# Optimization experiments

Measured on AMD Instinct MI355X. Metric: run time of the kernel, lower is better.

Reference implementation:

```python
import jax, jax.numpy as jnp
import numpy as np

B, A, C, L, NH, SCALE = 1, 5, 64, 4, 8, 2
H = W = 24
S = 2 * C
KS = 5


def layernorm(x, g, b, eps=1e-5):
    m = x.mean(-1, keepdims=True)
    v = ((x - m) ** 2).mean(-1, keepdims=True)
    return (x - m) * jax.lax.rsqrt(v + eps) * g + b


def pe_1d(n, d):
    # PositionEncoding: temperature**(2*(i//2)/d), sin of even cols then cos of odd cols
    g = jnp.arange(d, dtype=jnp.float32)
    g = 10000.0 ** (2.0 * jnp.floor(g / 2.0) / d)
    p = jnp.arange(n, dtype=jnp.float32)[:, None] / g[None, :]
    return jnp.concatenate([jnp.sin(p[:, 0::2]), jnp.cos(p[:, 1::2])], axis=1)  # [n, d]


def mha(qk, v, in_w, out_w, nh, mask=None):
    # qk, v: [Lq, Bt, D]; torch nn.MultiheadAttention, bias-free, q=k=qk, value=v
    Lq, Bt, D = qk.shape
    dh = D // nh
    wq, wk, wv = jnp.split(in_w, 3, axis=0)
    q = (qk @ wq.T).reshape(Lq, Bt, nh, dh)
    k = (qk @ wk.T).reshape(Lq, Bt, nh, dh)
    vv = (v @ wv.T).reshape(Lq, Bt, nh, dh)
    s = jnp.einsum('lbhd,mbhd->bhlm', q, k) / jnp.sqrt(jnp.float32(dh))
    if mask is not None:
        s = s + mask
    a = jax.nn.softmax(s, axis=-1)
    o = jnp.einsum('bhlm,mbhd->lbhd', a, vv).reshape(Lq, Bt, D)
    return o @ out_w.T


def unfold3x3(x):
    # F.unfold(k=3, pad=1).permute(2,0,1): [N,c,h,w] -> [h*w, N, 9c] (c, kh, kw ordering)
    N, c, h, w = x.shape
    xp = jnp.pad(x, ((0, 0), (0, 0), (1, 1), (1, 1)))
    p = jnp.stack([xp[:, :, i:i + h, j:j + w] for i in range(3) for j in range(3)], axis=2)
    return p.reshape(N, c * 9, h * w).transpose(2, 0, 1)


def conv_hw(x5, w):
    # Conv3d kernel (1,3,3) pad (0,1,1): 2D conv per angular view
    Bc, Ci, Aa, h, w_ = x5.shape
    y = jax.lax.conv_general_dilated(
        x5.transpose(0, 2, 1, 3, 4).reshape(Bc * Aa, Ci, h, w_), w, (1, 1), ((1, 1), (1, 1)),
        dimension_numbers=('NCHW', 'OIHW', 'NCHW'))
    return y.reshape(Bc, Aa, w.shape[0], h, w_).transpose(0, 2, 1, 3, 4)


def window_mask(h, w, k):
    # SpaTrans.gen_mask: additive -inf outside a k x k local window
    kl, kr = k // 2, k - k // 2
    i = jnp.arange(h)
    j = jnp.arange(w)
    mh = (i[None, :] >= i[:, None] - kl) & (i[None, :] < i[:, None] + kr)
    mw = (j[None, :] >= j[:, None] - kl) & (j[None, :] < j[:, None] + kr)
    m = (mh[:, None, :, None] & mw[None, :, None, :]).reshape(h * w, h * w)
    return jnp.where(m, 0.0, -jnp.inf).astype(jnp.float32)


def setup_inputs() -> dict:
    key = jax.random.key(0)
    ks = iter(jax.random.split(key, 64))
    def nrm(shape, s=0.02):
        return jax.random.normal(next(ks), shape, dtype=jnp.float32) * s
    d = {}
    d['lr'] = jax.random.normal(next(ks), (B, 1, A * H, A * W), dtype=jnp.float32)
    Hh, Wh = H * SCALE, W * SCALE
    ch = -1.0 + (2.0 * jnp.arange(Hh, dtype=jnp.float32) + 1.0) / Hh
    cw = -1.0 + (2.0 * jnp.arange(Wh, dtype=jnp.float32) + 1.0) / Wh
    g = jnp.stack(jnp.meshgrid(ch, cw, indexing='ij'), axis=-1).reshape(-1, 2)
    d['coord'] = jnp.broadcast_to(g, (B, Hh * Wh, 2))
    d['conv0_w'] = nrm((C, 1, 3, 3), 0.1)
    d['convi_w'] = nrm((3, C, C, 3, 3), 0.05)
    d['ang_ln_g'] = jnp.ones((L, C)); d['ang_ln_b'] = jnp.zeros((L, C))
    d['ang_in'] = nrm((L, 3 * C, C)); d['ang_out'] = nrm((L, C, C))
    d['ang_ff_g'] = jnp.ones((L, C)); d['ang_ff_b'] = jnp.zeros((L, C))
    d['ang_w1'] = nrm((L, 2 * C, C)); d['ang_w2'] = nrm((L, C, 2 * C))
    d['spa_mlp'] = nrm((L, S, 9 * C))
    d['spa_ln_g'] = jnp.ones((L, S)); d['spa_ln_b'] = jnp.zeros((L, S))
    d['spa_in'] = nrm((L, 3 * S, S)); d['spa_out'] = nrm((L, S, S))
    d['spa_ff_g'] = jnp.ones((L, S)); d['spa_ff_b'] = jnp.zeros((L, S))
    d['spa_w1'] = nrm((L, 2 * S, S)); d['spa_w2'] = nrm((L, S, 2 * S))
    d['spa_lin'] = nrm((L, C, S))
    IN = A * A * C + 2 + 2 * A * A
    d['imp_w0'] = nrm((320, IN)); d['imp_b0'] = jnp.zeros((320,))
    d['imp_w1'] = nrm((320, 320)); d['imp_b1'] = jnp.zeros((320,))
    d['imp_w2'] = nrm((3 * A * A, 320)); d['imp_b2'] = jnp.zeros((3 * A * A,))
    return d


def reference(lr, coord, conv0_w, convi_w, ang_ln_g, ang_ln_b, ang_in, ang_out,
              ang_ff_g, ang_ff_b, ang_w1, ang_w2, spa_mlp, spa_ln_g, spa_ln_b,
              spa_in, spa_out, spa_ff_g, spa_ff_b, spa_w1, spa_w2, spa_lin,
              imp_w0, imp_b0, imp_w1, imp_b1, imp_w2, imp_b2):
    Bn = lr.shape[0]
    # 'b c (a1 h) (a2 w) -> b c (a1 a2) h w'
    x = lr.reshape(Bn, 1, A, H, A, W).transpose(0, 1, 2, 4, 3, 5).reshape(Bn, 1, A * A, H, W)
    spa_pe_img = ((pe_1d(H, C)[:, None, :] + pe_1d(W, C)[None, :, :]) * 0.5).transpose(2, 0, 1)[None]  # [1,C,h,w]
    ang_pe = pe_1d(A * A, C)[:, None, :]  # [A^2,1,C]
    buf = conv_hw(x, conv0_w)
    t = buf
    for i in range(3):
        t = jax.nn.leaky_relu(conv_hw(t, convi_w[i]), 0.2)
    buf = t + buf
    mask = window_mask(H, W, KS)
    blk = buf
    for l in range(L):
        # ---- AngTrans: tokens [A^2, B*h*w, C]
        tok = blk.transpose(2, 0, 3, 4, 1).reshape(A * A, Bn * H * W, C)
        tn = layernorm(tok + ang_pe, ang_ln_g[l], ang_ln_b[l])
        tok = mha(tn, tok, ang_in[l], ang_out[l], NH) + tok
        ff = layernorm(tok, ang_ff_g[l], ang_ff_b[l])
        tok = jax.nn.relu(ff @ ang_w1[l].T) @ ang_w2[l].T + tok
        blk = tok.reshape(A * A, Bn, H, W, C).transpose(1, 4, 0, 2, 3)
        # ---- SpaTrans: tokens [h*w, B*A^2, 2C] with local-window mask
        xb = blk.transpose(0, 2, 1, 3, 4).reshape(Bn * A * A, C, H, W)
        tok = unfold3x3(xb) @ spa_mlp[l].T
        pe_tok = unfold3x3(spa_pe_img) @ spa_mlp[l].T
        tn = layernorm(tok + pe_tok, spa_ln_g[l], spa_ln_b[l])
        tok = mha(tn, tok, spa_in[l], spa_out[l], NH, mask) + tok
        ff = layernorm(tok, spa_ff_g[l], spa_ff_b[l])
        tok = jax.nn.relu(ff @ spa_w1[l].T) @ spa_w2[l].T + tok
        t5 = tok.reshape(H, W, Bn, A * A, S).transpose(2, 4, 3, 0, 1)  # b s a h w
        blk = jnp.einsum('os,bsahw->boahw', spa_lin[l], t5)  # 1x1x1 Conv3d
    buf = blk + buf
    # 'b c (a1 a2) h w -> b c (a1 h) (a2 w)'
    feat_lr = buf.reshape(Bn, C, A, A, H, W).transpose(0, 1, 2, 4, 3, 5).reshape(Bn, C, A * H, A * W)
    Hh, Wh = H * SCALE, W * SCALE
    # per-view bilinear upsample (align_corners=False)
    v = feat_lr.reshape(Bn, C, A, H, A, W).transpose(0, 2, 4, 1, 3, 5).reshape(Bn * A * A, C, H, W)
    v = jax.image.resize(v, (Bn * A * A, C, Hh, Wh), method='bilinear')
    feat_hr = v.reshape(Bn, A, A, C, Hh, Wh).transpose(0, 4, 5, 1, 2, 3).reshape(Bn, Hh, Wh, A * A * C)
    # nearest grid_sample of LR cell-center coords -> relative coord
    c_ = jnp.clip(coord + 1e-6, -1 + 1e-6, 1 - 1e-6)
    ih = jnp.clip(jnp.round(((c_[..., 0] + 1) * H - 1) / 2), 0, H - 1)
    iw = jnp.clip(jnp.round(((c_[..., 1] + 1) * W - 1) / 2), 0, W - 1)
    qh = -1.0 + (2.0 * ih + 1.0) / H
    qw = -1.0 + (2.0 * iw + 1.0) / W
    rel = jnp.stack([(coord[..., 0] - qh) * H, (coord[..., 1] - qw) * W], axis=-1).reshape(Bn, Hh, Wh, 2)
    au = 0.5 + jnp.arange(A, dtype=jnp.float32)  # make_coord ranges [0,A]
    ca = jnp.stack(jnp.meshgrid(au, au, indexing='ij'), axis=-1).reshape(-1)
    ca = jnp.broadcast_to(ca, (Bn, Hh, Wh, 2 * A * A))
    inp = jnp.concatenate([feat_hr, rel, ca], axis=-1)
    h0 = jax.nn.relu(inp @ imp_w0.T + imp_b0)
    h1 = jax.nn.relu(h0 @ imp_w1.T + imp_b1)
    o = h1 @ imp_w2.T + imp_b2
    # 'b h w (a1 a2 c) -> b c (a1 h) (a2 w)', c=3
    return o.reshape(Bn, Hh, Wh, A, A, 3).transpose(0, 5, 3, 1, 4, 2).reshape(Bn, 3, A * Hh, A * Wh)
```

## Files before the change

kernel.cpp:

```cpp
#include <hip/hip_runtime.h>
#include <math.h>

typedef short  s16x4 __attribute__((ext_vector_type(4)));
typedef short  s16x8 __attribute__((ext_vector_type(8)));
typedef float  f32x4 __attribute__((ext_vector_type(4)));

static const size_t PE25_  = 0;
static const size_t SPAPE_ = 2048;
static const size_t X_     = 38912;
static const size_t CAV_   = 53312;
static const size_t PETOK_ = 54272;
static const size_t W9C_   = 349184;
static const size_t W9S_   = 459776;
static const size_t BUF_   = 754688;
static const size_t BLK_   = 1676288;
static const size_t ATOK_  = 2597888;
static const size_t TNF_   = 3519488;
static const size_t STOK_  = 4441088;
static const size_t STOK2_ = 6284288;
static const size_t AO_    = 8127488;
static const size_t QKV_   = 9970688;
static const size_t WS_FLOATS = 15500288;
static const size_t T0_ = QKV_ + 2764800;
static const size_t T1_ = T0_ + 921600;
static const size_t ZP_ = QKV_;
static const size_t H0_ = STOK_;
static const size_t H1_ = STOK2_;

__device__ inline ushort f2bf(float x) {
  unsigned u = __float_as_uint(x);
  u += 0x7fffu + ((u >> 16) & 1u);
  return (ushort)(u >> 16);
}
__device__ inline float bf2f(ushort h) { return __uint_as_float(((unsigned)h) << 16); }

__device__ inline void store_split(char* p, f32x4 v) {
  s16x4 hi, lo;
  #pragma unroll
  for (int e = 0; e < 4; ++e) {
    float x = v[e];
    ushort h = f2bf(x);
    ushort l = f2bf(x - bf2f(h));
    hi[e] = (short)h; lo[e] = (short)l;
  }
  *(s16x4*)p = hi;
  *(s16x4*)(p + 1024) = lo;
}

__device__ inline void scatter_split(char* base, int rr, int c6, float v) {
  ushort hi = f2bf(v);
  ushort lo = f2bf(v - bf2f(hi));
  int ks = c6 >> 5, kh = (c6 >> 4) & 1, k4 = (c6 >> 2) & 3;
  int lane2 = (k4 >> 1)*32 + ((rr & 15) << 1) + (k4 & 1);
  int byt = (((rr >> 4)*2 + ks) << 11) + (kh << 9) + (lane2 << 3) + (c6 & 3)*2;
  *(ushort*)(base + byt) = hi;
  *(ushort*)(base + byt + 1024) = lo;
}

__device__ inline void ld_bf16x16(const ushort* p, float* dst) {
  s16x8 a = *(const s16x8*)p;
  s16x8 b = *(const s16x8*)(p + 8);
  #pragma unroll
  for (int e = 0; e < 8; ++e) { dst[e] = bf2f((ushort)a[e]); dst[8 + e] = bf2f((ushort)b[e]); }
}

__device__ inline void slot_decode(int i, int wave, int lane,
                                   int& row, int& kof, int& wo) {
  int idx = (i << 2) + wave;
  int msub = idx >> 2, ks = (idx >> 1) & 1, kh = idx & 1;
  int rsub = (lane >> 1) & 15;
  int ksub = ((lane >> 5) << 3) + ((lane & 1) << 2);
  row = (msub << 4) + rsub;
  kof = (ks << 5) + (kh << 4) + ksub;
  wo = ((msub * 2 + ks) << 11) + (kh << 9) + (lane << 3);
}

__device__ inline void mfma_step(const char* ldsA, const char* ldsB, int lane,
                                 int wr, int wc, f32x4 acc[2][2]) {
  #pragma unroll
  for (int ks = 0; ks < 2; ++ks) {
    s16x8 ah[2], al[2], bh[2], bl[2];
    #pragma unroll
    for (int i = 0; i < 2; ++i) {
      const char* pa = ldsA + (((wr*2 + i)*2 + ks) << 11) + (lane << 4);
      ah[i] = *(const s16x8*)pa;
      al[i] = *(const s16x8*)(pa + 1024);
      const char* pb = ldsB + (((wc*2 + i)*2 + ks) << 11) + (lane << 4);
      bh[i] = *(const s16x8*)pb;
      bl[i] = *(const s16x8*)(pb + 1024);
    }
    #pragma unroll
    for (int i = 0; i < 2; ++i) {
      #pragma unroll
      for (int j = 0; j < 2; ++j) {
        acc[i][j] = __builtin_amdgcn_mfma_f32_16x16x32_bf16(ah[i], bh[j], acc[i][j], 0, 0, 0);
        acc[i][j] = __builtin_amdgcn_mfma_f32_16x16x32_bf16(ah[i], bl[j], acc[i][j], 0, 0, 0);
        acc[i][j] = __builtin_amdgcn_mfma_f32_16x16x32_bf16(al[i], bh[j], acc[i][j], 0, 0, 0);
      }
    }
  }
}

__device__ inline void epilogue(f32x4 acc[2][2], const float* bias, const float* res,
                                float* out, int N, int m0, int n0,
                                int wr, int wc, int lane, int act) {
  int colb = n0 + wc*32 + (lane & 15);
  int rowb = m0 + wr*32 + ((lane >> 4) << 2);
  #pragma unroll
  for (int j = 0; j < 2; ++j) {
    int cc = colb + j*16;
    if (cc >= N) continue;
    float bv = bias ? bias[cc] : 0.f;
    #pragma unroll
    for (int i = 0; i < 2; ++i) {
      #pragma unroll
      for (int r = 0; r < 4; ++r) {
        int rr = rowb + i*16 + r;
        float v = acc[i][j][r] + bv;
        if (act == 1) v = fmaxf(v, 0.f);
        else if (act == 2) v = v > 0.f ? v : 0.2f*v;
        if (res) v += res[(long)rr*N + cc];
        if (act == 3) {
          int hh = rr / 48, ww2 = rr % 48, q = cc / 3, ch = cc % 3;
          out[ch*57600 + ((q/5)*48 + hh)*240 + (q%5)*48 + ww2] = v;
        } else if (act == 4) {
          ((ushort*)out)[(long)rr*N + cc] = f2bf(v);
        } else {
          out[(long)rr*N + cc] = v;
        }
      }
    }
  }
}

template<int K, int LN>
__global__ __launch_bounds__(256) void mgemm3_k(
    const float* __restrict__ A, const float* __restrict__ A2, int nsplit,
    const float* __restrict__ pe, int pe_mode,
    const float* __restrict__ g, const float* __restrict__ bb,
    const float* __restrict__ W, const float* __restrict__ bias,
    const float* __restrict__ res, float* __restrict__ out,
    int N, int act, int Mreal, int Mpad) {
  constexpr int NCH = K / 64;
  __shared__ char Apl[NCH * 16384];
  __shared__ char Bp[16384];
  __shared__ float sw_[4][64][2];
  __shared__ float sf_[64][2];
  int bid = blockIdx.x;
  int m = bid % Mpad, nt = bid / Mpad;
  if (m >= Mreal) return;
  int m0 = m*64, n0 = nt*64;
  int t = threadIdx.x, lane = t & 63, wave = t >> 6;
  int wr = wave >> 1, wc = wave & 1;
  bool use_norm = LN && (n0 < nsplit);

  if (LN && use_norm) {
    f32x4 rv[NCH][4];
    float sA[4], sQ[4];
    #pragma unroll
    for (int i = 0; i < 4; ++i) { sA[i] = 0.f; sQ[i] = 0.f; }
    #pragma unroll
    for (int ch = 0; ch < NCH; ++ch)
      #pragma unroll
      for (int i = 0; i < 4; ++i) {
        int row, kof, wo;
        slot_decode(i, wave, lane, row, kof, wo);
        int gk = ch*64 + kof;
        f32x4 av = *(const f32x4*)&A[(long)(m0 + row)*K + gk];
        if (pe_mode == 0)      av += *(const f32x4*)&pe[(long)(m0/576)*K + gk];
        else if (pe_mode == 1) av += *(const f32x4*)&pe[(long)(m0%576 + row)*K + gk];
        rv[ch][i] = av;
        #pragma unroll
        for (int e = 0; e < 4; ++e) { sA[i] += av[e]; sQ[i] = fmaf(av[e], av[e], sQ[i]); }
      }
    #pragma unroll
    for (int i = 0; i < 4; ++i) {
      float s = sA[i], q = sQ[i];
      s += __shfl_xor(s, 1, 64);  q += __shfl_xor(q, 1, 64);
      s += __shfl_xor(s, 32, 64); q += __shfl_xor(q, 32, 64);
      if ((lane & 1) == 0 && lane < 32) {
        int row = i*16 + (lane >> 1);
        sw_[wave][row][0] = s; sw_[wave][row][1] = q;
      }
    }
    __syncthreads();
    if (t < 64) {
      float s = sw_[0][t][0] + sw_[1][t][0] + sw_[2][t][0] + sw_[3][t][0];
      float q = sw_[0][t][1] + sw_[1][t][1] + sw_[2][t][1] + sw_[3][t][1];
      float mean = s / K, var = q / K - mean*mean;
      sf_[t][0] = mean; sf_[t][1] = rsqrtf(var + 1e-5f);
    }
    __syncthreads();
    #pragma unroll
    for (int ch = 0; ch < NCH; ++ch)
      #pragma unroll
      for (int i = 0; i < 4; ++i) {
        int row, kof, wo;
        slot_decode(i, wave, lane, row, kof, wo);
        int gk = ch*64 + kof;
        float mean = sf_[row][0], rstd = sf_[row][1];
        f32x4 gv = *(const f32x4*)&g[gk];
        f32x4 bv = *(const f32x4*)&bb[gk];
        f32x4 nv;
        #pragma unroll
        for (int e = 0; e < 4; ++e) nv[e] = (rv[ch][i][e] - mean)*rstd*gv[e] + bv[e];
        store_split(Apl + ch*16384 + wo, nv);
      }
  } else {
    const float* As = LN ? A2 : A;
    #pragma unroll
    for (int ch = 0; ch < NCH; ++ch)
      #pragma unroll
      for (int i = 0; i < 4; ++i) {
        int row, kof, wo;
        slot_decode(i, wave, lane, row, kof, wo);
        f32x4 av = *(const f32x4*)&As[(long)(m0 + row)*K + ch*64 + kof];
        store_split(Apl + ch*16384 + wo, av);
      }
  }

  f32x4 pb[4];
  #pragma unroll
  for (int i = 0; i < 4; ++i) {
    int row, kof, wo;
    slot_decode(i, wave, lane, row, kof, wo);
    int br = n0 + row;
    pb[i] = (br < N) ? *(const f32x4*)&W[(long)br*K + kof] : (f32x4){0.f,0.f,0.f,0.f};
  }
  __syncthreads();
  f32x4 acc[2][2];
  #pragma unroll
  for (int i = 0; i < 2; ++i)
    #pragma unroll
    for (int j = 0; j < 2; ++j) acc[i][j] = (f32x4){0.f,0.f,0.f,0.f};
  for (int ch = 0; ch < NCH; ++ch) {
    #pragma unroll
    for (int i = 0; i < 4; ++i) {
      int row, kof, wo;
      slot_decode(i, wave, lane, row, kof, wo);
      store_split(Bp + wo, pb[i]);
    }
    __syncthreads();
    if (ch + 1 < NCH) {
      #pragma unroll
      for (int i = 0; i < 4; ++i) {
        int row, kof, wo;
        slot_decode(i, wave, lane, row, kof, wo);
        int br = n0 + row;
        pb[i] = (br < N) ? *(const f32x4*)&W[(long)br*K + (ch+1)*64 + kof]
                         : (f32x4){0.f,0.f,0.f,0.f};
      }
    }
    mfma_step(Apl + ch*16384, Bp, lane, wr, wc, acc);
    if (ch + 1 < NCH) __syncthreads();
  }
  epilogue(acc, bias, res, out, N, m0, n0, wr, wc, lane, act);
}

__global__ __launch_bounds__(256) void cgemm3_k(
    const float* __restrict__ in, const float* __restrict__ W9, long wstride,
    const float* __restrict__ res, float* __restrict__ out, long ostride,
    int N, int act, int Mreal, int Mpad) {
  __shared__ float halo[144 * 68];
  __shared__ char Ap[16384], Bp[16384];
  int bid = blockIdx.x;
  int m = bid % Mpad, nt = bid / Mpad;
  if (m >= Mreal) return;
  int ly = blockIdx.y;
  W9  += (long)ly * wstride;
  out += (long)ly * ostride;
  int m0 = m*64, n0 = nt*64;
  int a = m0 / 576, off = m0 % 576;
  int h_lo = off/24 - 1, h_hi = (off + 63)/24 + 1;
  int RH = h_hi - h_lo + 1;
  int t = threadIdx.x, lane = t & 63, wave = t >> 6;
  int wr = wave >> 1, wc = wave & 1;
  for (int sidx = t; sidx < RH*24*16; sidx += 256) {
    int tokr = sidx >> 4, c4 = (sidx & 15) << 2;
    int h = h_lo + tokr/24, w = tokr % 24;
    f32x4 v = {0.f,0.f,0.f,0.f};
    if ((unsigned)h < 24u) v = *(const f32x4*)&in[(long)(a*576 + h*24 + w)*64 + c4];
    *(f32x4*)&halo[tokr*68 + c4] = v;
  }
  f32x4 pb[4];
  #pragma unroll
  for (int i = 0; i < 4; ++i) {
    int row, kof, wo;
    slot_decode(i, wave, lane, row, kof, wo);
    int br = n0 + row;
    pb[i] = (br < N) ? *(const f32x4*)&W9[(long)br*64 + kof] : (f32x4){0.f,0.f,0.f,0.f};
  }
  __syncthreads();
  f32x4 acc[2][2];
  #pragma unroll
  for (int i = 0; i < 2; ++i)
    #pragma unroll
    for (int j = 0; j < 2; ++j) acc[i][j] = (f32x4){0.f,0.f,0.f,0.f};
  for (int ij = 0; ij < 9; ++ij) {
    int di = ij/3 - 1, dj = ij%3 - 1;
    #pragma unroll
    for (int i = 0; i < 4; ++i) {
      int row, kof, wo;
      slot_decode(i, wave, lane, row, kof, wo);
      int tok = off + row;
      int h2 = tok/24 + di, w2 = tok%24 + dj;
      f32x4 v = {0.f,0.f,0.f,0.f};
      if ((unsigned)h2 < 24u && (unsigned)w2 < 24u)
        v = *(const f32x4*)&halo[((h2 - h_lo)*24 + w2)*68 + kof];
      store_split(Ap + wo, v);
      store_split(Bp + wo, pb[i]);
    }
    __syncthreads();
    if (ij < 8) {
      #pragma unroll
      for (int i = 0; i < 4; ++i) {
        int row, kof, wo;
        slot_decode(i, wave, lane, row, kof, wo);
        int br = n0 + row;
        pb[i] = (br < N) ? *(const f32x4*)&W9[((long)(ij+1)*N + br)*64 + kof]
                         : (f32x4){0.f,0.f,0.f,0.f};
      }
    }
    mfma_step(Ap, Bp, lane, wr, wc, acc);
    if (ij < 8) __syncthreads();
  }
  epilogue(acc, nullptr, res, out, N, m0, n0, wr, wc, lane, act);
}

__global__ __launch_bounds__(256) void ang_mega_k(
    const ushort* __restrict__ qkv, const float* __restrict__ Wout,
    const float* __restrict__ blkr, const float* __restrict__ g,
    const float* __restrict__ bb, float* __restrict__ atok, float* __restrict__ tnf) {
  int hw = blockIdx.x;
  __shared__ float lq[25*192];
  __shared__ float lao[25*64];
  __shared__ float po[25*68];
  __shared__ float wout[64*65];
  __shared__ float st[25][2];
  int t = threadIdx.x;
  for (int idx = t; idx < 600; idx += 256) {
    int a3 = idx / 24, c8 = (idx % 24) * 8;
    s16x8 r = *(const s16x8*)&qkv[(long)(a3*576 + hw)*192 + c8];
    #pragma unroll
    for (int e = 0; e < 8; ++e) lq[a3*192 + c8 + e] = bf2f((ushort)r[e]);
  }
  for (int idx = t; idx < 4096; idx += 256) {
    int c = idx >> 6, d = idx & 63;
    wout[c*65 + d] = Wout[idx];
  }
  __syncthreads();
  if (t < 200) {
    int l = t / 8, head = t & 7;
    const float* q = lq + l*192 + head*8;
    float s[25]; float mx = -1e30f;
    #pragma unroll
    for (int mm = 0; mm < 25; ++mm) {
      const float* kk = lq + mm*192 + 64 + head*8;
      float acc = 0.f;
      #pragma unroll
      for (int d = 0; d < 8; ++d) acc = fmaf(q[d], kk[d], acc);
      acc *= 0.3535533905932738f;
      s[mm] = acc; mx = fmaxf(mx, acc);
    }
    float sum = 0.f;
    #pragma unroll
    for (int mm = 0; mm < 25; ++mm) { s[mm] = expf(s[mm] - mx); sum += s[mm]; }
    float inv = 1.f / sum;
    #pragma unroll
    for (int d = 0; d < 8; ++d) {
      float acc = 0.f;
      #pragma unroll
      for (int mm = 0; mm < 25; ++mm) acc = fmaf(s[mm], lq[mm*192 + 128 + head*8 + d], acc);
      lao[l*64 + head*8 + d] = acc * inv;
    }
  }
  __syncthreads();
  for (int idx = t; idx < 1600; idx += 256) {
    int tok = idx >> 6, c = idx & 63;
    const float* ar = &lao[tok*64];
    const float* wr = &wout[c*65];
    float accp = 0.f;
    #pragma unroll 16
    for (int d = 0; d < 64; ++d) accp = fmaf(ar[d], wr[d], accp);
    po[tok*68 + c] = accp + blkr[(long)(tok*576 + hw)*64 + c];
  }
  __syncthreads();
  if (t < 25) {
    float s = 0.f, q = 0.f;
    for (int c = 0; c < 64; ++c) { float x = po[t*68 + c]; s += x; q = fmaf(x, x, q); }
    float mean = s / 64.f, var = q / 64.f - mean*mean;
    st[t][0] = mean; st[t][1] = rsqrtf(var + 1e-5f);
  }
  __syncthreads();
  for (int idx = t; idx < 1600; idx += 256) {
    int tok = idx >> 6, c = idx & 63;
    float x = po[tok*68 + c];
    long gidx = (long)(tok*576 + hw)*64 + c;
    atok[gidx] = x;
    tnf[gidx] = (x - st[tok][0]) * st[tok][1] * g[c] + bb[c];
  }
}

__global__ __launch_bounds__(256) void ffn_ang_k(
    const float* __restrict__ tnf, const float* __restrict__ w1,
    const float* __restrict__ w2, float* __restrict__ atok,
    int Mreal, int Mpad) {
  __shared__ char Ap[16384], Bp[16384], Hp[2][16384];
  int bid = blockIdx.x;
  int m = bid % Mpad;
  if (m >= Mreal) return;
  int m0 = m*64;
  int t = threadIdx.x, lane = t & 63, wave = t >> 6;
  int wr = wave >> 1, wc = wave & 1;
  #pragma unroll
  for (int i = 0; i < 4; ++i) {
    int row, kof, wo;
    slot_decode(i, wave, lane, row, kof, wo);
    f32x4 av = *(const f32x4*)&tnf[(long)(m0 + row)*64 + kof];
    store_split(Ap + wo, av);
  }
  f32x4 pb[4];
  #pragma unroll
  for (int i = 0; i < 4; ++i) {
    int row, kof, wo;
    slot_decode(i, wave, lane, row, kof, wo);
    pb[i] = *(const f32x4*)&w1[(long)row*64 + kof];
  }
  __syncthreads();
  for (int nt = 0; nt < 2; ++nt) {
    #pragma unroll
    for (int i = 0; i < 4; ++i) {
      int row, kof, wo;
      slot_decode(i, wave, lane, row, kof, wo);
      store_split(Bp + wo, pb[i]);
    }
    __syncthreads();
    #pragma unroll
    for (int i = 0; i < 4; ++i) {
      int row, kof, wo;
      slot_decode(i, wave, lane, row, kof, wo);
      pb[i] = (nt == 0) ? *(const f32x4*)&w1[(long)(64 + row)*64 + kof]
                        : *(const f32x4*)&w2[(long)row*128 + kof];
    }
    f32x4 acc[2][2];
    #pragma unroll
    for (int i = 0; i < 2; ++i)
      #pragma unroll
      for (int j = 0; j < 2; ++j) acc[i][j] = (f32x4){0.f,0.f,0.f,0.f};
    mfma_step(Ap, Bp, lane, wr, wc, acc);
    #pragma unroll
    for (int jj = 0; jj < 2; ++jj)
      #pragma unroll
      for (int ii = 0; ii < 2; ++ii)
        #pragma unroll
        for (int r = 0; r < 4; ++r) {
          int rr = wr*32 + ii*16 + ((lane >> 4) << 2) + r;
          int cc = wc*32 + jj*16 + (lane & 15);
          scatter_split(Hp[nt], rr, cc, fmaxf(acc[ii][jj][r], 0.f));
        }
    __syncthreads();
  }
  f32x4 acc2[2][2];
  #pragma unroll
  for (int i = 0; i < 2; ++i)
    #pragma unroll
    for (int j = 0; j < 2; ++j) acc2[i][j] = (f32x4){0.f,0.f,0.f,0.f};
  for (int ch = 0; ch < 2; ++ch) {
    #pragma unroll
    for (int i = 0; i < 4; ++i) {
      int row, kof, wo;
      slot_decode(i, wave, lane, row, kof, wo);
      store_split(Bp + wo, pb[i]);
    }
    __syncthreads();
    if (ch == 0) {
      #pragma unroll
      for (int i = 0; i < 4; ++i) {
        int row, kof, wo;
        slot_decode(i, wave, lane, row, kof, wo);
        pb[i] = *(const f32x4*)&w2[(long)row*128 + 64 + kof];
      }
    }
    mfma_step(Hp[ch], Bp, lane, wr, wc, acc2);
    if (ch == 0) __syncthreads();
  }
  epilogue(acc2, nullptr, atok, atok, 64, m0, 0, wr, wc, lane, 0);
}

__global__ __launch_bounds__(512) void megaspa_k(
    const ushort* __restrict__ qkv, const float* __restrict__ stok,
    const float* __restrict__ wout, const float* __restrict__ g,
    const float* __restrict__ bb, const float* __restrict__ w1,
    const float* __restrict__ w2, const float* __restrict__ wlin,
    float* __restrict__ outb, int Mreal, int Mpad) {
  __shared__ char Aop[32768];
  __shared__ char Bp2[2][16384];
  __shared__ char Hp2[2][16384];
  __shared__ float Rf[64*132];
  __shared__ float st[64][2];
  int bid = blockIdx.x;
  int m = bid % Mpad;
  if (m >= Mreal) return;
  int m0 = m*64;
  int t = threadIdx.x, lane = t & 63, wave = t >> 6;
  int wgrp = wave >> 2, w4 = wave & 3;
  int wr = w4 >> 1, wc = w4 & 1;
  char* Bp = Bp2[wgrp];

  for (int idx = t; idx < 2048; idx += 512) {
    int row = idx >> 5, c4 = (idx & 31) << 2;
    *(f32x4*)&Rf[row*132 + c4] = *(const f32x4*)&stok[(long)(m0 + row)*128 + c4];
  }

  {
    int rr = t >> 3, head = t & 7;
    int x = m0 + rr;
    int hw = x % 576, h = hw / 24, w = hw % 24;
    float qr[16];
    ld_bf16x16(qkv + (long)x*384 + head*16, qr);
    float s[25]; float mx = -1e30f;
    #pragma unroll
    for (int ro = 0; ro < 5; ++ro) {
      int h2 = h + ro - 2;
      s16x8 k0[5], k1[5];
      #pragma unroll
      for (int co = 0; co < 5; ++co) {
        int xt = x + (ro - 2)*24 + (co - 2);
        xt = min(max(xt, 0), 14399);
        const ushort* kp = qkv + (long)xt*384 + 128 + head*16;
        k0[co] = *(const s16x8*)kp;
        k1[co] = *(const s16x8*)(kp + 8);
      }
      #pragma unroll
      for (int co = 0; co < 5; ++co) {
        int w2c = w + co - 2;
        float sc = -1e30f;
        if (h2 >= 0 && h2 < 24 && w2c >= 0 && w2c < 24) {
          sc = 0.f;
          #pragma unroll
          for (int d = 0; d < 8; ++d) sc = fmaf(qr[d], bf2f((ushort)k0[co][d]), sc);
          #pragma unroll
          for (int d = 0; d < 8; ++d) sc = fmaf(qr[8+d], bf2f((ushort)k1[co][d]), sc);
          sc *= 0.25f;
        }
        s[ro*5 + co] = sc; mx = fmaxf(mx, sc);
      }
    }
    float sum = 0.f;
    #pragma unroll
    for (int i = 0; i < 25; ++i) {
      float e = (s[i] > -1e29f) ? expf(s[i] - mx) : 0.f;
      s[i] = e; sum += e;
    }
    float inv = 1.f / sum;
    float acc[16];
    #pragma unroll
    for (int d = 0; d < 16; ++d) acc[d] = 0.f;
    #pragma unroll
    for (int ro = 0; ro < 5; ++ro) {
      s16x8 v0[5], v1[5];
      #pragma unroll
      for (int co = 0; co < 5; ++co) {
        int xt = x + (ro - 2)*24 + (co - 2);
        xt = min(max(xt, 0), 14399);
        const ushort* vp = qkv + (long)xt*384 + 256 + head*16;
        v0[co] = *(const s16x8*)vp;
        v1[co] = *(const s16x8*)(vp + 8);
      }
      #pragma unroll
      for (int co = 0; co < 5; ++co) {
        float sv = s[ro*5 + co];
        #pragma unroll
        for (int d = 0; d < 8; ++d) acc[d] = fmaf(sv, bf2f((ushort)v0[co][d]), acc[d]);
        #pragma unroll
        for (int d = 0; d < 8; ++d) acc[8+d] = fmaf(sv, bf2f((ushort)v1[co][d]), acc[8+d]);
      }
    }
    #pragma unroll
    for (int d = 0; d < 16; ++d) {
      int cc = head*16 + d;
      scatter_split(Aop + (cc >> 6)*16384, rr, cc & 63, acc[d] * inv);
    }
  }

  {
    int nt = wgrp;
    f32x4 acc[2][2];
    #pragma unroll
    for (int i = 0; i < 2; ++i)
      #pragma unroll
      for (int j = 0; j < 2; ++j) acc[i][j] = (f32x4){0.f,0.f,0.f,0.f};
    for (int ch = 0; ch < 2; ++ch) {
      __syncthreads();
      #pragma unroll
      for (int i = 0; i < 4; ++i) {
        int row, kof, wo;
        slot_decode(i, w4, lane, row, kof, wo);
        f32x4 bv = *(const f32x4*)&wout[(long)(nt*64 + row)*128 + ch*64 + kof];
        store_split(Bp + wo, bv);
      }
      __syncthreads();
      mfma_step(Aop + ch*16384, Bp, lane, wr, wc, acc);
    }
    int colb = nt*64 + wc*32 + (lane & 15);
    int rowb = wr*32 + ((lane >> 4) << 2);
    #pragma unroll
    for (int j = 0; j < 2; ++j)
      #pragma unroll
      for (int i = 0; i < 2; ++i)
        #pragma unroll
        for (int r = 0; r < 4; ++r) {
          int rr = rowb + i*16 + r, cc = colb + j*16;
          Rf[rr*132 + cc] += acc[i][j][r];
        }
  }
  __syncthreads();

  {
    int row = t >> 3, q8 = t & 7;
    const float* yr = &Rf[row*132 + q8*16];
    float s = 0.f, sq = 0.f;
    #pragma unroll
    for (int j2 = 0; j2 < 16; ++j2) { float xv = yr[j2]; s += xv; sq = fmaf(xv, xv, sq); }
    s += __shfl_xor(s, 1, 64); sq += __shfl_xor(sq, 1, 64);
    s += __shfl_xor(s, 2, 64); sq += __shfl_xor(sq, 2, 64);
    s += __shfl_xor(s, 4, 64); sq += __shfl_xor(sq, 4, 64);
    if (q8 == 0) {
      float mean = s / 128.f, var = sq / 128.f - mean*mean;
      st[row][0] = mean; st[row][1] = rsqrtf(var + 1e-5f);
    }
  }
  __syncthreads();
  {
    int ch = wgrp;
    #pragma unroll
    for (int i = 0; i < 4; ++i) {
      int row, kof, wo;
      slot_decode(i, w4, lane, row, kof, wo);
      int gk = ch*64 + kof;
      f32x4 xv = *(const f32x4*)&Rf[row*132 + gk];
      float mean = st[row][0], rstd = st[row][1];
      f32x4 gv = *(const f32x4*)&g[gk];
      f32x4 bv = *(const f32x4*)&bb[gk];
      f32x4 nv;
      #pragma unroll
      for (int e = 0; e < 4; ++e) nv[e] = (xv[e] - mean)*rstd*gv[e] + bv[e];
      store_split(Aop + ch*16384 + wo, nv);
    }
  }

  f32x4 acc2[2][2];
  #pragma unroll
  for (int i = 0; i < 2; ++i)
    #pragma unroll
    for (int j = 0; j < 2; ++j) acc2[i][j] = (f32x4){0.f,0.f,0.f,0.f};
  for (int r = 0; r < 2; ++r) {
    int nt = 2*r + wgrp;
    f32x4 accH[2][2];
    #pragma unroll
    for (int i = 0; i < 2; ++i)
      #pragma unroll
      for (int j = 0; j < 2; ++j) accH[i][j] = (f32x4){0.f,0.f,0.f,0.f};
    for (int ch = 0; ch < 2; ++ch) {
      __syncthreads();
      #pragma unroll
      for (int i = 0; i < 4; ++i) {
        int row, kof, wo;
        slot_decode(i, w4, lane, row, kof, wo);
        f32x4 bv = *(const f32x4*)&w1[(long)(nt*64 + row)*128 + ch*64 + kof];
        store_split(Bp + wo, bv);
      }
      __syncthreads();
      mfma_step(Aop + ch*16384, Bp, lane, wr, wc, accH);
    }
    #pragma unroll
    for (int jj = 0; jj < 2; ++jj)
      #pragma unroll
      for (int ii = 0; ii < 2; ++ii)
        #pragma unroll
        for (int rx = 0; rx < 4; ++rx) {
          int rr = wr*32 + ii*16 + ((lane >> 4) << 2) + rx;
          int cc = wc*32 + jj*16 + (lane & 15);
          scatter_split(Hp2[wgrp], rr, cc, fmaxf(accH[ii][jj][rx], 0.f));
        }
    for (int q = 0; q < 2; ++q) {
      __syncthreads();
      #pragma unroll
      for (int i = 0; i < 4; ++i) {
        int row, kof, wo;
        slot_decode(i, w4, lane, row, kof, wo);
        f32x4 bv = *(const f32x4*)&w2[(long)(wgrp*64 + row)*256 + (2*r + q)*64 + kof];
        store_split(Bp + wo, bv);
      }
      __syncthreads();
      mfma_step(Hp2[q], Bp, lane, wr, wc, acc2);
    }
  }
  {
    int colb = wc*32 + (lane & 15);
    int rowb = wr*32 + ((lane >> 4) << 2);
    #pragma unroll
    for (int jj = 0; jj < 2; ++jj)
      #pragma unroll
      for (int ii = 0; ii < 2; ++ii)
        #pragma unroll
        for (int rx = 0; rx < 4; ++rx) {
          int rr = rowb + ii*16 + rx;
          int cc = colb + jj*16;
          scatter_split(Aop + wgrp*16384, rr, cc,
                        acc2[ii][jj][rx] + Rf[rr*132 + wgrp*64 + cc]);
        }
  }

  f32x4 acc3[2][2];
  #pragma unroll
  for (int i = 0; i < 2; ++i)
    #pragma unroll
    for (int j = 0; j < 2; ++j) acc3[i][j] = (f32x4){0.f,0.f,0.f,0.f};
  for (int ch = 0; ch < 2; ++ch) {
    __syncthreads();
    if (wgrp == 0) {
      #pragma unroll
      for (int i = 0; i < 4; ++i) {
        int row, kof, wo;
        slot_decode(i, w4, lane, row, kof, wo);
        f32x4 bv = *(const f32x4*)&wlin[(long)row*128 + ch*64 + kof];
        store_split(Bp2[0] + wo, bv);
      }
    }
    __syncthreads();
    if (wgrp == 0) mfma_step(Aop + ch*16384, Bp2[0], lane, wr, wc, acc3);
  }
  if (wgrp == 0)
    epilogue(acc3, nullptr, nullptr, outb, 64, m0, 0, wr, wc, lane, 0);
}

__global__ __launch_bounds__(256) void zgemm3_k(
    const float* __restrict__ buf, const float* __restrict__ blk,
    const float* __restrict__ W0, float* __restrict__ Zp) {
  __shared__ char Ap[16384], Bp[16384];
  int bid = blockIdx.x;
  int m = bid % 16; if (m >= 9) return;
  int nz = bid / 16;
  int n = nz % 5, z = nz / 5;
  int m0 = m*64, n0 = n*64;
  int t = threadIdx.x, lane = t & 63, wave = t >> 6;
  int wr = wave >> 1, wc = wave & 1;
  f32x4 pa[4], pb[4];
  #pragma unroll
  for (int i = 0; i < 4; ++i) {
    int row, kof, wo;
    slot_decode(i, wave, lane, row, kof, wo);
    long tok = (long)(z*5)*576 + m0 + row;
    pa[i] = *(const f32x4*)&buf[tok*64 + kof];
    pa[i] += *(const f32x4*)&blk[tok*64 + kof];
    pb[i] = *(const f32x4*)&W0[(long)(n0 + row)*1652 + (z*5)*64 + kof];
  }
  f32x4 acc[2][2];
  #pragma unroll
  for (int i = 0; i < 2; ++i)
    #pragma unroll
    for (int j = 0; j < 2; ++j) acc[i][j] = (f32x4){0.f,0.f,0.f,0.f};
  for (int q = 0; q < 5; ++q) {
    #pragma unroll
    for (int i = 0; i < 4; ++i) {
      int row, kof, wo;
      slot_decode(i, wave, lane, row, kof, wo);
      store_split(Ap + wo, pa[i]);
      store_split(Bp + wo, pb[i]);
    }
    __syncthreads();
    if (q < 4) {
      #pragma unroll
      for (int i = 0; i < 4; ++i) {
        int row, kof, wo;
        slot_decode(i, wave, lane, row, kof, wo);
        long tok = (long)(z*5 + q + 1)*576 + m0 + row;
        pa[i] = *(const f32x4*)&buf[tok*64 + kof];
        pa[i] += *(const f32x4*)&blk[tok*64 + kof];
        pb[i] = *(const f32x4*)&W0[(long)(n0 + row)*1652 + (z*5 + q + 1)*64 + kof];
      }
    }
    mfma_step(Ap, Bp, lane, wr, wc, acc);
    if (q < 4) __syncthreads();
  }
  epilogue(acc, nullptr, nullptr, Zp + (long)z*184320, 320, m0, n0, wr, wc, lane, 0);
}

__global__ void combine_k(const float* __restrict__ Zp, const float* __restrict__ cav,
                          const float* __restrict__ coord, float* __restrict__ h0out) {
  int gidx = blockIdx.x * 256 + threadIdx.x;
  if (gidx >= 2304 * 320) return;
  int p = gidx / 320, o = gidx % 320;
  int hh = p / 48, ww = p % 48;
  float sh = hh * 0.5f - 0.25f, sw = ww * 0.5f - 0.25f;
  int h0i = (int)floorf(sh); float fh = sh - h0i;
  int w0i = (int)floorf(sw); float fw = sw - w0i;
  int h0c = max(h0i, 0), h1c = min(h0i + 1, 23);
  int w0c = max(w0i, 0), w1c = min(w0i + 1, 23);
  int i00 = (h0c*24 + w0c)*320 + o, i01 = (h0c*24 + w1c)*320 + o;
  int i10 = (h1c*24 + w0c)*320 + o, i11 = (h1c*24 + w1c)*320 + o;
  float z00 = 0.f, z01 = 0.f, z10 = 0.f, z11 = 0.f;
  #pragma unroll
  for (int z = 0; z < 5; ++z) {
    const float* Zz = Zp + (long)z*184320;
    z00 += Zz[i00]; z01 += Zz[i01]; z10 += Zz[i10]; z11 += Zz[i11];
  }
  float v = (1.f-fh)*((1.f-fw)*z00 + fw*z01) + fh*((1.f-fw)*z10 + fw*z11);
  #pragma unroll
  for (int d = 0; d < 2; ++d) {
    float co = coord[p*2 + d];
    float cc = fminf(fmaxf(co + 1e-6f, -1.f + 1e-6f), 1.f - 1e-6f);
    float ix = rintf(((cc + 1.f)*24.f - 1.f)*0.5f);
    ix = fminf(fmaxf(ix, 0.f), 23.f);
    float q = -1.f + (2.f*ix + 1.f)/24.f;
    v = fmaf((co - q)*24.f, cav[320*(d+1) + o], v);
  }
  h0out[gidx] = fmaxf(v + cav[o], 0.f);
}

__device__ inline float pe_val(int pos, int c) {
  int j = c & 31;
  float freq = powf(10000.f, -2.f * (float)j / 64.f);
  float arg = (float)pos * freq;
  return (c < 32) ? sinf(arg) : cosf(arg);
}

__global__ void setup_k(const float* __restrict__ lr, const float* __restrict__ convi_w,
                        const float* __restrict__ spa_mlp,
                        const float* __restrict__ imp_w0, const float* __restrict__ imp_b0,
                        float* pe25, float* spa_pe, float* X, float* w9c, float* w9s,
                        float* cav) {
  int g = blockIdx.x * 256 + threadIdx.x;
  if (g < 1600) { pe25[g] = pe_val(g >> 6, g & 63); return; }
  g -= 1600;
  if (g < 36864) {
    int hw = g >> 6, c = g & 63; int h = hw / 24, w = hw % 24;
    spa_pe[g] = 0.5f * (pe_val(h, c) + pe_val(w, c)); return;
  }
  g -= 36864;
  if (g < 14400) {
    int aa = g / 576, hw = g % 576, h = hw / 24, w = hw % 24;
    X[g] = lr[((aa/5)*24 + h)*120 + (aa%5)*24 + w]; return;
  }
  g -= 14400;
  if (g < 110592) {
    int cv = g / 36864, rem = g % 36864;
    int ij = rem / 4096, oc = rem % 4096;
    int o = oc >> 6, c = oc & 63;
    w9c[g] = convi_w[((long)(cv*64 + o)*64 + c)*9 + ij]; return;
  }
  g -= 110592;
  if (g < 294912) {
    int l = g / 73728, rem = g % 73728;
    int ij = rem / 8192, oc = rem % 8192;
    int o = oc >> 6, c = oc & 63;
    w9s[g] = spa_mlp[((long)(l*128 + o))*576 + c*9 + ij]; return;
  }
  g -= 294912;
  if (g < 320) {
    int o = g;
    float s = imp_b0[o];
    #pragma unroll
    for (int idx = 0; idx < 50; ++idx) {
      int pair = idx >> 1;
      float cvv = 0.5f + (float)((idx & 1) ? pair % 5 : pair / 5);
      s = fmaf(cvv, imp_w0[(long)o*1652 + 1602 + idx], s);
    }
    cav[o] = s;
    cav[320 + o] = imp_w0[(long)o*1652 + 1600];
    cav[640 + o] = imp_w0[(long)o*1652 + 1601];
  }
}

__global__ void conv0_k(const float* __restrict__ X, const float* __restrict__ W,
                        float* __restrict__ out) {
  int sp = threadIdx.x >> 6, lane = threadIdx.x & 63;
  int strip = blockIdx.x * 4 + sp;
  int a = strip / 48, r = strip % 48, h = r >> 1, w0 = (r & 1) * 12;
  __shared__ float patch[4][3][16];
  if (lane < 42) {
    int i = lane / 14, col = lane % 14;
    int h2 = h + i - 1, w2 = w0 + col - 1;
    float v = 0.f;
    if ((unsigned)h2 < 24u && (unsigned)w2 < 24u) v = X[a*576 + h2*24 + w2];
    patch[sp][i][col] = v;
  }
  __syncthreads();
  float wv[9];
  #pragma unroll
  for (int q = 0; q < 9; ++q) wv[q] = W[lane*9 + q];
  #pragma unroll
  for (int p = 0; p < 12; ++p) {
    float acc = 0.f;
    #pragma unroll
    for (int i = 0; i < 3; ++i)
      #pragma unroll
      for (int j = 0; j < 3; ++j)
        acc = fmaf(patch[sp][i][p + j], wv[i*3 + j], acc);
    out[(long)(a*576 + h*24 + w0 + p)*64 + lane] = acc;
  }
}

extern "C" void kernel_launch(void* const* d_in, const int* in_sizes, int n_in,
                              void* d_out, int out_size, void* d_ws, size_t ws_size,
                              hipStream_t stream) {
  (void)in_sizes; (void)n_in; (void)out_size;
  if (ws_size < (size_t)WS_FLOATS * 4) return;
  float* ws = (float*)d_ws;

  const float* lr       = (const float*)d_in[0];
  const float* coord    = (const float*)d_in[1];
  const float* conv0_w  = (const float*)d_in[2];
  const float* convi_w  = (const float*)d_in[3];
  const float* ang_ln_g = (const float*)d_in[4];
  const float* ang_ln_b = (const float*)d_in[5];
  const float* ang_in   = (const float*)d_in[6];
  const float* ang_out  = (const float*)d_in[7];
  const float* ang_ff_g = (const float*)d_in[8];
  const float* ang_ff_b = (const float*)d_in[9];
  const float* ang_w1   = (const float*)d_in[10];
  const float* ang_w2   = (const float*)d_in[11];
  const float* spa_mlp  = (const float*)d_in[12];
  const float* spa_ln_g = (const float*)d_in[13];
  const float* spa_ln_b = (const float*)d_in[14];
  const float* spa_in   = (const float*)d_in[15];
  const float* spa_out  = (const float*)d_in[16];
  const float* spa_ff_g = (const float*)d_in[17];
  const float* spa_ff_b = (const float*)d_in[18];
  const float* spa_w1   = (const float*)d_in[19];
  const float* spa_w2   = (const float*)d_in[20];
  const float* spa_lin  = (const float*)d_in[21];
  const float* imp_w0   = (const float*)d_in[22];
  const float* imp_b0   = (const float*)d_in[23];
  const float* imp_w1   = (const float*)d_in[24];
  const float* imp_b1   = (const float*)d_in[25];
  const float* imp_w2   = (const float*)d_in[26];
  const float* imp_b2   = (const float*)d_in[27];

  float* pe25 = ws + PE25_;  float* spa_pe = ws + SPAPE_;  float* X = ws + X_;
  float* cav = ws + CAV_;    float* petok = ws + PETOK_;
  float* w9c = ws + W9C_;    float* w9s = ws + W9S_;
  float* buf = ws + BUF_;    float* blk = ws + BLK_;      float* atok = ws + ATOK_;
  float* tnf = ws + TNF_;    float* stok = ws + STOK_;
  float* qkvf = ws + QKV_;   ushort* qkvh = (ushort*)(ws + QKV_);
  float* t0 = ws + T0_;      float* t1 = ws + T1_;
  float* Zp = ws + ZP_;      float* h0 = ws + H0_;        float* h1 = ws + H1_;

  setup_k<<<1792, 256, 0, stream>>>(lr, convi_w, spa_mlp, imp_w0, imp_b0,
                                    pe25, spa_pe, X, w9c, w9s, cav);
  conv0_k<<<300, 256, 0, stream>>>(X, conv0_w, buf);
  cgemm3_k<<<dim3(232,1), 256, 0, stream>>>(buf, w9c,         0, nullptr, t0,  0, 64, 2, 225, 232);
  cgemm3_k<<<dim3(232,1), 256, 0, stream>>>(t0,  w9c + 36864, 0, nullptr, t1,  0, 64, 2, 225, 232);
  cgemm3_k<<<dim3(232,1), 256, 0, stream>>>(t1,  w9c + 73728, 0, buf,     buf, 0, 64, 2, 225, 232);
  cgemm3_k<<<dim3(32, 4), 256, 0, stream>>>(spa_pe, w9s, 73728, nullptr, petok, 73728,
                                            128, 0, 9, 16);

  for (int l = 0; l < 4; ++l) {
    const float* blkr = (l == 0) ? buf : blk;
    mgemm3_k<64,1><<<696, 256, 0, stream>>>(blkr, blkr, 128, pe25, 0,
        ang_ln_g + l*64, ang_ln_b + l*64, ang_in + l*192*64, nullptr, nullptr,
        qkvf, 192, 4, 225, 232);
    ang_mega_k<<<576, 256, 0, stream>>>(qkvh, ang_out + l*64*64, blkr,
        ang_ff_g + l*64, ang_ff_b + l*64, atok, tnf);
    ffn_ang_k<<<232, 256, 0, stream>>>(tnf, ang_w1 + l*128*64, ang_w2 + l*64*128,
        atok, 225, 232);
    cgemm3_k<<<dim3(464,1), 256, 0, stream>>>(atok, w9s + l*73728, 0, nullptr, stok, 0,
        128, 0, 225, 232);
    mgemm3_k<128,1><<<1392, 256, 0, stream>>>(stok, stok, 256, petok + l*73728, 1,
        spa_ln_g + l*128, spa_ln_b + l*128, spa_in + l*384*128, nullptr, nullptr,
        qkvf, 384, 4, 225, 232);
    megaspa_k<<<232, 512, 0, stream>>>(qkvh, stok, spa_out + l*128*128,
        spa_ff_g + l*128, spa_ff_b + l*128, spa_w1 + l*256*128, spa_w2 + l*128*256,
        spa_lin + l*64*128, blk, 225, 232);
  }

  zgemm3_k<<<400, 256, 0, stream>>>(buf, blk, imp_w0, Zp);
  combine_k<<<2880, 256, 0, stream>>>(Zp, cav, coord, h0);
  mgemm3_k<320,0><<<200, 256, 0, stream>>>(h0, h0, 0, nullptr, -1, nullptr, nullptr,
      imp_w1, imp_b1, nullptr, h1, 320, 1, 36, 40);
  mgemm3_k<320,0><<<80, 256, 0, stream>>>(h1, h1, 0, nullptr, -1, nullptr, nullptr,
      imp_w2, imp_b2, nullptr, (float*)d_out, 75, 3, 36, 40);
}
```

Measured before the change: 598.5 us.

## Stage window K/V rows in shared memory for local spatial attention

The spatial windowed attention in megaspa_k now cooperatively loads the K and then the V rows covering the block's 64 tokens plus a 2-row halo into LDS, in padded rows. Each thread then reads its 5x5 neighbourhood from shared memory instead of issuing 25 scattered global loads per pass. The LDS buffers for B and H operands are merged into one scratch region that is reused for the K/V tiles. zgemm3_k's grid is also shrunk so no blocks exit early. This adds two extra barriers and a staging pass, and the larger LDS footprint per block may reduce occupancy.

New measurement: 601.9 us. About the same (+0.6%).

```diff
diff --git a/kernel.cpp b/kernel.cpp
--- a/kernel.cpp
+++ b/kernel.cpp
@@ -494,8 +494,7 @@
     const float* __restrict__ w2, const float* __restrict__ wlin,
     float* __restrict__ outb, int Mreal, int Mpad) {
   __shared__ char Aop[32768];
-  __shared__ char Bp2[2][16384];
-  __shared__ char Hp2[2][16384];
+  __shared__ char SCR[65536];
   __shared__ float Rf[64*132];
   __shared__ float st[64][2];
   int bid = blockIdx.x;
@@ -505,81 +504,101 @@
   int t = threadIdx.x, lane = t & 63, wave = t >> 6;
   int wgrp = wave >> 2, w4 = wave & 3;
   int wr = w4 >> 1, wc = w4 & 1;
-  char* Bp = Bp2[wgrp];
+  char* Bp  = SCR + wgrp*16384;
+  char* Hp0 = SCR + 32768;
+  char* Hp1 = SCR + 49152;
+  ushort* KV = (ushort*)SCR;
 
   for (int idx = t; idx < 2048; idx += 512) {
     int row = idx >> 5, c4 = (idx & 31) << 2;
     *(f32x4*)&Rf[row*132 + c4] = *(const f32x4*)&stok[(long)(m0 + row)*128 + c4];
   }
 
+  int va = m0 / 576, off = m0 % 576;
+  int hb = off/24 - 2;
+  int he = (off + 63)/24 + 2;
+  int RH = he - hb + 1;
+  int rr1 = t >> 3, head = t & 7;
+  int x = m0 + rr1;
+  int hw = x % 576, h = hw / 24, w = hw % 24;
+  float qr[16];
+  ld_bf16x16(qkv + (long)x*384 + head*16, qr);
+  for (int idx = t; idx < RH*24*16; idx += 512) {
+    int tokr = idx >> 4, c8 = (idx & 15) << 3;
+    int hh2 = hb + tokr/24, ww2 = tokr % 24;
+    s16x8 vv = (s16x8){0,0,0,0,0,0,0,0};
+    if ((unsigned)hh2 < 24u)
+      vv = *(const s16x8*)&qkv[(long)(va*576 + hh2*24 + ww2)*384 + 128 + c8];
+    *(s16x8*)&KV[tokr*136 + c8] = vv;
+  }
+  __syncthreads();
+  float s[25]; float mx = -1e30f;
+  #pragma unroll
+  for (int ro = 0; ro < 5; ++ro) {
+    int h2 = h + ro - 2;
+    int hrow = h2 - hb;
+    #pragma unroll
+    for (int co = 0; co < 5; ++co) {
+      int w2 = w + co - 2;
+      int w2c = min(max(w2, 0), 23);
+      const ushort* kp = &KV[(hrow*24 + w2c)*136 + head*16];
+      s16x8 k0 = *(const s16x8*)kp;
+      s16x8 k1 = *(const s16x8*)(kp + 8);
+      float sc = -1e30f;
+      if (h2 >= 0 && h2 < 24 && w2 >= 0 && w2 < 24) {
+        sc = 0.f;
+        #pragma unroll
+        for (int d = 0; d < 8; ++d) sc = fmaf(qr[d], bf2f((ushort)k0[d]), sc);
+        #pragma unroll
+        for (int d = 0; d < 8; ++d) sc = fmaf(qr[8+d], bf2f((ushort)k1[d]), sc);
+        sc *= 0.25f;
+      }
+      s[ro*5 + co] = sc; mx = fmaxf(mx, sc);
+    }
+  }
+  float sum = 0.f;
+  #pragma unroll
+  for (int i = 0; i < 25; ++i) {
+    float e = (s[i] > -1e29f) ? expf(s[i] - mx) : 0.f;
+    s[i] = e; sum += e;
+  }
+  float inv = 1.f / sum;
+  __syncthreads();
+  for (int idx = t; idx < RH*24*16; idx += 512) {
+    int tokr = idx >> 4, c8 = (idx & 15) << 3;
+    int hh2 = hb + tokr/24, ww2 = tokr % 24;
+    s16x8 vv = (s16x8){0,0,0,0,0,0,0,0};
+    if ((unsigned)hh2 < 24u)
+      vv = *(const s16x8*)&qkv[(long)(va*576 + hh2*24 + ww2)*384 + 256 + c8];
+    *(s16x8*)&KV[tokr*136 + c8] = vv;
+  }
+  __syncthreads();
   {
-    int rr = t >> 3, head = t & 7;
-    int x = m0 + rr;
-    int hw = x % 576, h = hw / 24, w = hw % 24;
-    float qr[16];
-    ld_bf16x16(qkv + (long)x*384 + head*16, qr);
-    float s[25]; float mx = -1e30f;
+    float acc[16];
+    #pragma unroll
+    for (int d = 0; d < 16; ++d) acc[d] = 0.f;
     #pragma unroll
     for (int ro = 0; ro < 5; ++ro) {
       int h2 = h + ro - 2;
-      s16x8 k0[5], k1[5];
+      int hrow = h2 - hb;
       #pragma unroll
       for (int co = 0; co < 5; ++co) {
-        int xt = x + (ro - 2)*24 + (co - 2);
-        xt = min(max(xt, 0), 14399);
-        const ushort* kp = qkv + (long)xt*384 + 128 + head*16;
-        k0[co] = *(const s16x8*)kp;
-        k1[co] = *(const s16x8*)(kp + 8);
-      }
-      #pragma unroll
-      for (int co = 0; co < 5; ++co) {
-        int w2c = w + co - 2;
-        float sc = -1e30f;
-        if (h2 >= 0 && h2 < 24 && w2c >= 0 && w2c < 24) {
-          sc = 0.f;
-          #pragma unroll
-          for (int d = 0; d < 8; ++d) sc = fmaf(qr[d], bf2f((ushort)k0[co][d]), sc);
-          #pragma unroll
-          for (int d = 0; d < 8; ++d) sc = fmaf(qr[8+d], bf2f((ushort)k1[co][d]), sc);
-          sc *= 0.25f;
-        }
-        s[ro*5 + co] = sc; mx = fmaxf(mx, sc);
-      }
-    }
-    float sum = 0.f;
-    #pragma unroll
-    for (int i = 0; i < 25; ++i) {
-      float e = (s[i] > -1e29f) ? expf(s[i] - mx) : 0.f;
-      s[i] = e; sum += e;
-    }
-    float inv = 1.f / sum;
-    float acc[16];
-    #pragma unroll
-    for (int d = 0; d < 16; ++d) acc[d] = 0.f;
-    #pragma unroll
-    for (int ro = 0; ro < 5; ++ro) {
-      s16x8 v0[5], v1[5];
-      #pragma unroll
-      for (int co = 0; co < 5; ++co) {
-        int xt = x + (ro - 2)*24 + (co - 2);
-        xt = min(max(xt, 0), 14399);
-        const ushort* vp = qkv + (long)xt*384 + 256 + head*16;
-        v0[co] = *(const s16x8*)vp;
-        v1[co] = *(const s16x8*)(vp + 8);
-      }
-      #pragma unroll
-      for (int co = 0; co < 5; ++co) {
+        int w2 = w + co - 2;
+        int w2c = min(max(w2, 0), 23);
+        const ushort* vp = &KV[(hrow*24 + w2c)*136 + head*16];
+        s16x8 v0 = *(const s16x8*)vp;
+        s16x8 v1 = *(const s16x8*)(vp + 8);
         float sv = s[ro*5 + co];
         #pragma unroll
-        for (int d = 0; d < 8; ++d) acc[d] = fmaf(sv, bf2f((ushort)v0[co][d]), acc[d]);
+        for (int d = 0; d < 8; ++d) acc[d] = fmaf(sv, bf2f((ushort)v0[d]), acc[d]);
         #pragma unroll
-        for (int d = 0; d < 8; ++d) acc[8+d] = fmaf(sv, bf2f((ushort)v1[co][d]), acc[8+d]);
+        for (int d = 0; d < 8; ++d) acc[8+d] = fmaf(sv, bf2f((ushort)v1[d]), acc[8+d]);
       }
     }
     #pragma unroll
     for (int d = 0; d < 16; ++d) {
       int cc = head*16 + d;
-      scatter_split(Aop + (cc >> 6)*16384, rr, cc & 63, acc[d] * inv);
+      scatter_split(Aop + (cc >> 6)*16384, rr1, cc & 63, acc[d] * inv);
     }
   }
 
@@ -619,14 +638,14 @@
   {
     int row = t >> 3, q8 = t & 7;
     const float* yr = &Rf[row*132 + q8*16];
-    float s = 0.f, sq = 0.f;
-    #pragma unroll
-    for (int j2 = 0; j2 < 16; ++j2) { float xv = yr[j2]; s += xv; sq = fmaf(xv, xv, sq); }
-    s += __shfl_xor(s, 1, 64); sq += __shfl_xor(sq, 1, 64);
-    s += __shfl_xor(s, 2, 64); sq += __shfl_xor(sq, 2, 64);
-    s += __shfl_xor(s, 4, 64); sq += __shfl_xor(sq, 4, 64);
+    float sm = 0.f, sq = 0.f;
+    #pragma unroll
+    for (int j2 = 0; j2 < 16; ++j2) { float xv = yr[j2]; sm += xv; sq = fmaf(xv, xv, sq); }
+    sm += __shfl_xor(sm, 1, 64); sq += __shfl_xor(sq, 1, 64);
+    sm += __shfl_xor(sm, 2, 64); sq += __shfl_xor(sq, 2, 64);
+    sm += __shfl_xor(sm, 4, 64); sq += __shfl_xor(sq, 4, 64);
     if (q8 == 0) {
-      float mean = s / 128.f, var = sq / 128.f - mean*mean;
+      float mean = sm / 128.f, var = sq / 128.f - mean*mean;
       st[row][0] = mean; st[row][1] = rsqrtf(var + 1e-5f);
     }
   }
@@ -673,6 +692,7 @@
       __syncthreads();
       mfma_step(Aop + ch*16384, Bp, lane, wr, wc, accH);
     }
+    char* Hpw = wgrp ? Hp1 : Hp0;
     #pragma unroll
     for (int jj = 0; jj < 2; ++jj)
       #pragma unroll
@@ -681,7 +701,7 @@
         for (int rx = 0; rx < 4; ++rx) {
           int rr = wr*32 + ii*16 + ((lane >> 4) << 2) + rx;
           int cc = wc*32 + jj*16 + (lane & 15);
-          scatter_split(Hp2[wgrp], rr, cc, fmaxf(accH[ii][jj][rx], 0.f));
+          scatter_split(Hpw, rr, cc, fmaxf(accH[ii][jj][rx], 0.f));
         }
     for (int q = 0; q < 2; ++q) {
       __syncthreads();
@@ -693,7 +713,7 @@
         store_split(Bp + wo, bv);
       }
       __syncthreads();
-      mfma_step(Hp2[q], Bp, lane, wr, wc, acc2);
+      mfma_step(q ? Hp1 : Hp0, Bp, lane, wr, wc, acc2);
     }
   }
   {
@@ -725,11 +745,11 @@
         int row, kof, wo;
         slot_decode(i, w4, lane, row, kof, wo);
         f32x4 bv = *(const f32x4*)&wlin[(long)row*128 + ch*64 + kof];
-        store_split(Bp2[0] + wo, bv);
+        store_split(SCR + wo, bv);
       }
     }
     __syncthreads();
-    if (wgrp == 0) mfma_step(Aop + ch*16384, Bp2[0], lane, wr, wc, acc3);
+    if (wgrp == 0) mfma_step(Aop + ch*16384, SCR, lane, wr, wc, acc3);
   }
   if (wgrp == 0)
     epilogue(acc3, nullptr, nullptr, outb, 64, m0, 0, wr, wc, lane, 0);
@@ -740,8 +760,8 @@
     const float* __restrict__ W0, float* __restrict__ Zp) {
   __shared__ char Ap[16384], Bp[16384];
   int bid = blockIdx.x;
-  int m = bid % 16; if (m >= 9) return;
-  int nz = bid / 16;
+  int m = bid % 9;
+  int nz = bid / 9;
   int n = nz % 5, z = nz / 5;
   int m0 = m*64, n0 = n*64;
   int t = threadIdx.x, lane = t & 63, wave = t >> 6;
@@ -975,7 +995,7 @@
         spa_lin + l*64*128, blk, 225, 232);
   }
 
-  zgemm3_k<<<400, 256, 0, stream>>>(buf, blk, imp_w0, Zp);
+  zgemm3_k<<<225, 256, 0, stream>>>(buf, blk, imp_w0, Zp);
   combine_k<<<2880, 256, 0, stream>>>(Zp, cav, coord, h0);
   mgemm3_k<320,0><<<200, 256, 0, stream>>>(h0, h0, 0, nullptr, -1, nullptr, nullptr,
       imp_w1, imp_b1, nullptr, h1, 320, 1, 36, 40);
```
